# Performance work log

Hardware: AMD Instinct MI355X
Metric: run time of the kernel (lower is better)

The kernel has to match this reference:

```python
import jax, jax.numpy as jnp
import numpy as np

N_CAPS = 64
CAPS_DIM = 16
OUTPUT_DIM = 128
ITERATIONS = 3
P = 1152
BATCH = 256


def squash(x):
    # norm over last dim; scale = norm / (1 + norm^2)
    norm = jnp.linalg.norm(x, axis=-1, keepdims=True)
    scale = norm / (1.0 + norm * norm)
    return scale * x


def setup_inputs() -> dict:
    key = jax.random.key(0)
    kx, kw = jax.random.split(key)
    x = jax.random.normal(kx, (P, BATCH, OUTPUT_DIM), dtype=jnp.float32)
    caps_weights = 0.01 * jax.random.normal(kw, (N_CAPS, CAPS_DIM, OUTPUT_DIM), dtype=jnp.float32)
    return {"x": x, "caps_weights": caps_weights}


def reference(x, caps_weights):
    # 'n c o, p b o -> b n o': sums over c (caps_dim) and p simultaneously
    xp = jnp.einsum('nco,pbo->bno', caps_weights, x)  # (B, N, O)
    x_det = jax.lax.stop_gradient(xp)
    b = xp.shape[0]
    logits = jnp.zeros((b, 1, N_CAPS), dtype=xp.dtype)
    coeffs = jax.nn.softmax(logits, axis=-1)
    for _ in range(ITERATIONS - 1):
        routed = squash(coeffs @ x_det)                 # (B, 1, O)
        logits = logits + routed @ jnp.swapaxes(x_det, -1, -2)  # (B, 1, N)
        coeffs = jax.nn.softmax(logits, axis=-1)
    return squash(coeffs @ xp)                          # (B, 1, O)
```

## Files before the change

kernel.cpp:

```cpp
#include <hip/hip_runtime.h>
#include <math.h>

#define NB 256
#define NO 128
#define NC 64
#define CD 16
#define PP 1152
#define BO (NB*NO)
#define BO4 (BO/4)

template<int PT>
__global__ __launch_bounds__(256) void psum_kernel(const float4* __restrict__ x4,
                                                   float4* __restrict__ part4,
                                                   const float* __restrict__ cw,
                                                   float* __restrict__ Wg) {
    if ((int)blockIdx.y == PP / PT) {
        int idx = blockIdx.x * 256 + threadIdx.x;
        int n = idx >> 7, o = idx & 127;
        float acc = 0.f;
        #pragma unroll
        for (int c = 0; c < CD; ++c) acc += cw[n * CD * NO + c * NO + o];
        Wg[idx] = acc;
        return;
    }
    int bo4 = blockIdx.x * 256 + threadIdx.x;
    const float4* p = x4 + (size_t)(blockIdx.y * PT) * BO4 + bo4;
    float ax = 0.f, ay = 0.f, az = 0.f, aw = 0.f;
    #pragma unroll
    for (int i = 0; i < PT; ++i) {
        float4 v = p[(size_t)i * BO4];
        ax += v.x; ay += v.y; az += v.z; aw += v.w;
    }
    part4[(size_t)blockIdx.y * BO4 + bo4] = make_float4(ax, ay, az, aw);
}

template<int NP>
__global__ __launch_bounds__(256) void route_kernel(const float4* __restrict__ part4,
                                                    const float* __restrict__ Wg,
                                                    float* __restrict__ out) {
    __shared__ float  W_s[NC][NO + 1];
    __shared__ float4 S_red4[8][32];
    __shared__ float  S_s[NO];
    __shared__ float  routed_s[NO];
    __shared__ float  logits_s[NC];
    __shared__ float  coeffs_s[NC];
    __shared__ float  red[2];

    const int t = threadIdx.x;
    const int b = blockIdx.x;
    const int lane = t & 63, wid = t >> 6;

    for (int i = t; i < NC * NO; i += 256) W_s[i >> 7][i & 127] = Wg[i];

    {
        int o4 = t & 31, jc = t >> 5;
        float4 a = make_float4(0.f, 0.f, 0.f, 0.f);
        for (int j = jc; j < NP; j += 8) {
            float4 v = part4[(size_t)j * BO4 + b * 32 + o4];
            a.x += v.x; a.y += v.y; a.z += v.z; a.w += v.w;
        }
        S_red4[jc][o4] = a;
    }
    if (t < NC) { logits_s[t] = 0.f; coeffs_s[t] = 1.f / 64.f; }
    __syncthreads();

    float s = 0.f;
    if (t < 128) {
        const float* sr = (const float*)S_red4;
        #pragma unroll
        for (int jc = 0; jc < 8; ++jc) s += sr[jc * 128 + t];
        S_s[t] = s;
    }
    __syncthreads();

    for (int it = 0; it < 2; ++it) {
        float v = 0.f;
        if (t < 128) {
            #pragma unroll
            for (int n = 0; n < NC; ++n) v += coeffs_s[n] * W_s[n][t];
            v *= s;
            float v2 = v * v;
            #pragma unroll
            for (int m = 32; m >= 1; m >>= 1) v2 += __shfl_xor(v2, m, 64);
            if (lane == 0) red[wid] = v2;
        }
        __syncthreads();
        if (t < 128) {
            float nv = red[0] + red[1];
            float scale = sqrtf(nv) / (1.f + nv);
            routed_s[t] = scale * v;
        }
        __syncthreads();
        if (t < NC) {
            float acc = 0.f;
            #pragma unroll 8
            for (int oo = 0; oo < NO; ++oo)
                acc += routed_s[oo] * W_s[t][oo] * S_s[oo];
            float lg = logits_s[t] + acc;
            logits_s[t] = lg;
            float mx = lg;
            #pragma unroll
            for (int m = 32; m >= 1; m >>= 1) mx = fmaxf(mx, __shfl_xor(mx, m, 64));
            float e = expf(lg - mx);
            float Z = e;
            #pragma unroll
            for (int m = 32; m >= 1; m >>= 1) Z += __shfl_xor(Z, m, 64);
            coeffs_s[t] = e / Z;
        }
        __syncthreads();
    }

    float v = 0.f;
    if (t < 128) {
        #pragma unroll
        for (int n = 0; n < NC; ++n) v += coeffs_s[n] * W_s[n][t];
        v *= s;
        float v2 = v * v;
        #pragma unroll
        for (int m = 32; m >= 1; m >>= 1) v2 += __shfl_xor(v2, m, 64);
        if (lane == 0) red[wid] = v2;
    }
    __syncthreads();
    if (t < 128) {
        float nv = red[0] + red[1];
        float scale = sqrtf(nv) / (1.f + nv);
        out[b * NO + t] = scale * v;
    }
}

extern "C" void kernel_launch(void* const* d_in, const int* in_sizes, int n_in,
                              void* d_out, int out_size, void* d_ws, size_t ws_size,
                              hipStream_t stream) {
    const float* x  = (const float*)d_in[0];
    const float* cw = (const float*)d_in[1];
    float* out = (float*)d_out;
    float* part = (float*)d_ws;

    const size_t need48 = (size_t)(PP / 48) * BO * sizeof(float) + (size_t)NC * NO * sizeof(float);
    if (ws_size >= need48) {
        float* Wg = part + (size_t)(PP / 48) * BO;
        psum_kernel<48><<<dim3(32, PP / 48 + 1), 256, 0, stream>>>(
            (const float4*)x, (float4*)part, cw, Wg);
        route_kernel<24><<<dim3(NB), 256, 0, stream>>>((const float4*)part, Wg, out);
    } else {
        float* Wg = part + (size_t)(PP / 128) * BO;
        psum_kernel<128><<<dim3(32, PP / 128 + 1), 256, 0, stream>>>(
            (const float4*)x, (float4*)part, cw, Wg);
        route_kernel<9><<<dim3(NB), 256, 0, stream>>>((const float4*)part, Wg, out);
    }
}
```

Measured before the change: 219.3 us.

## Fuse P-reduction and weight summation into single per-batch routing kernel

Replaces the two-kernel pipeline (partial sums over P into a workspace, then routing) with one 512-thread kernel per batch element. Each block reads its own 512-byte slice of x across all 1152 P rows and reduces it on chip, and it also recomputes the caps-dim weight sum into shared memory. This removes the workspace round trip and one launch. In exchange only 256 blocks stream the 151 MB input with strided 512-byte accesses, and every block redundantly re-reads the 512 KB weight tensor.

```diff
diff --git a/kernel.cpp b/kernel.cpp
--- a/kernel.cpp
+++ b/kernel.cpp
@@ -6,40 +6,13 @@
 #define NC 64
 #define CD 16
 #define PP 1152
-#define BO (NB*NO)
-#define BO4 (BO/4)
+#define BO4 8192
 
-template<int PT>
-__global__ __launch_bounds__(256) void psum_kernel(const float4* __restrict__ x4,
-                                                   float4* __restrict__ part4,
-                                                   const float* __restrict__ cw,
-                                                   float* __restrict__ Wg) {
-    if ((int)blockIdx.y == PP / PT) {
-        int idx = blockIdx.x * 256 + threadIdx.x;
-        int n = idx >> 7, o = idx & 127;
-        float acc = 0.f;
-        #pragma unroll
-        for (int c = 0; c < CD; ++c) acc += cw[n * CD * NO + c * NO + o];
-        Wg[idx] = acc;
-        return;
-    }
-    int bo4 = blockIdx.x * 256 + threadIdx.x;
-    const float4* p = x4 + (size_t)(blockIdx.y * PT) * BO4 + bo4;
-    float ax = 0.f, ay = 0.f, az = 0.f, aw = 0.f;
-    #pragma unroll
-    for (int i = 0; i < PT; ++i) {
-        float4 v = p[(size_t)i * BO4];
-        ax += v.x; ay += v.y; az += v.z; aw += v.w;
-    }
-    part4[(size_t)blockIdx.y * BO4 + bo4] = make_float4(ax, ay, az, aw);
-}
-
-template<int NP>
-__global__ __launch_bounds__(256) void route_kernel(const float4* __restrict__ part4,
-                                                    const float* __restrict__ Wg,
-                                                    float* __restrict__ out) {
+__global__ __launch_bounds__(512) void capsule_kernel(const float4* __restrict__ x4,
+                                                      const float4* __restrict__ cw4,
+                                                      float* __restrict__ out) {
     __shared__ float  W_s[NC][NO + 1];
-    __shared__ float4 S_red4[8][32];
+    __shared__ float4 S_red4[16][32];
     __shared__ float  S_s[NO];
     __shared__ float  routed_s[NO];
     __shared__ float  logits_s[NC];
@@ -48,34 +21,49 @@
 
     const int t = threadIdx.x;
     const int b = blockIdx.x;
+    const int o4 = t & 31, pc = t >> 5;
     const int lane = t & 63, wid = t >> 6;
 
-    for (int i = t; i < NC * NO; i += 256) W_s[i >> 7][i & 127] = Wg[i];
+    {
+        const float4* p = x4 + (size_t)pc * BO4 + b * 32 + o4;
+        float ax = 0.f, ay = 0.f, az = 0.f, aw = 0.f;
+        #pragma unroll 8
+        for (int j = 0; j < PP / 16; ++j) {
+            float4 v = p[(size_t)j * 16 * BO4];
+            ax += v.x; ay += v.y; az += v.z; aw += v.w;
+        }
+        S_red4[pc][o4] = make_float4(ax, ay, az, aw);
+    }
 
-    {
-        int o4 = t & 31, jc = t >> 5;
+    #pragma unroll
+    for (int k = 0; k < 4; ++k) {
+        int idx = t + k * 512;
+        int n = idx >> 5, oq = idx & 31;
         float4 a = make_float4(0.f, 0.f, 0.f, 0.f);
-        for (int j = jc; j < NP; j += 8) {
-            float4 v = part4[(size_t)j * BO4 + b * 32 + o4];
+        #pragma unroll
+        for (int c = 0; c < CD; ++c) {
+            float4 v = cw4[n * (CD * 32) + c * 32 + oq];
             a.x += v.x; a.y += v.y; a.z += v.z; a.w += v.w;
         }
-        S_red4[jc][o4] = a;
+        W_s[n][4 * oq + 0] = a.x; W_s[n][4 * oq + 1] = a.y;
+        W_s[n][4 * oq + 2] = a.z; W_s[n][4 * oq + 3] = a.w;
     }
+
     if (t < NC) { logits_s[t] = 0.f; coeffs_s[t] = 1.f / 64.f; }
     __syncthreads();
 
     float s = 0.f;
-    if (t < 128) {
+    if (t < NO) {
         const float* sr = (const float*)S_red4;
         #pragma unroll
-        for (int jc = 0; jc < 8; ++jc) s += sr[jc * 128 + t];
+        for (int j = 0; j < 16; ++j) s += sr[j * 128 + t];
         S_s[t] = s;
     }
     __syncthreads();
 
     for (int it = 0; it < 2; ++it) {
         float v = 0.f;
-        if (t < 128) {
+        if (t < NO) {
             #pragma unroll
             for (int n = 0; n < NC; ++n) v += coeffs_s[n] * W_s[n][t];
             v *= s;
@@ -85,7 +73,7 @@
             if (lane == 0) red[wid] = v2;
         }
         __syncthreads();
-        if (t < 128) {
+        if (t < NO) {
             float nv = red[0] + red[1];
             float scale = sqrtf(nv) / (1.f + nv);
             routed_s[t] = scale * v;
@@ -111,7 +99,7 @@
     }
 
     float v = 0.f;
-    if (t < 128) {
+    if (t < NO) {
         #pragma unroll
         for (int n = 0; n < NC; ++n) v += coeffs_s[n] * W_s[n][t];
         v *= s;
@@ -121,7 +109,7 @@
         if (lane == 0) red[wid] = v2;
     }
     __syncthreads();
-    if (t < 128) {
+    if (t < NO) {
         float nv = red[0] + red[1];
         float scale = sqrtf(nv) / (1.f + nv);
         out[b * NO + t] = scale * v;
@@ -134,18 +122,5 @@
     const float* x  = (const float*)d_in[0];
     const float* cw = (const float*)d_in[1];
     float* out = (float*)d_out;
-    float* part = (float*)d_ws;
-
-    const size_t need48 = (size_t)(PP / 48) * BO * sizeof(float) + (size_t)NC * NO * sizeof(float);
-    if (ws_size >= need48) {
-        float* Wg = part + (size_t)(PP / 48) * BO;
-        psum_kernel<48><<<dim3(32, PP / 48 + 1), 256, 0, stream>>>(
-            (const float4*)x, (float4*)part, cw, Wg);
-        route_kernel<24><<<dim3(NB), 256, 0, stream>>>((const float4*)part, Wg, out);
-    } else {
-        float* Wg = part + (size_t)(PP / 128) * BO;
-        psum_kernel<128><<<dim3(32, PP / 128 + 1), 256, 0, stream>>>(
-            (const float4*)x, (float4*)part, cw, Wg);
-        route_kernel<9><<<dim3(NB), 256, 0, stream>>>((const float4*)part, Wg, out);
-    }
+    capsule_kernel<<<dim3(NB), 512, 0, stream>>>((const float4*)x, (const float4*)cw, out);
 }
```

After: 216.9 us. About the same (-1.1%).
